# Performance work log

Measured on AMD Instinct MI355X. Metric: run time of the kernel, lower is better.

Reference implementation:

```python
import jax, jax.numpy as jnp
from jax import lax
import numpy as np

RATIOS = (0.5, 1.0, 2.0)
SCALES = (8, 16, 32)
BASE = 16
STRIDE = 16
IMG_H, IMG_W = 1024, 1024
NMS_THR = 0.7
N_IN = 6000   # eval mode (training=False)
N_OUT = 300
MIN_SIZE = 16


def _base_anchors():
    ctr = BASE / 2.0
    anc = []
    for r in RATIOS:
        for s in SCALES:
            h = BASE * s * np.sqrt(r)
            w = BASE * s * np.sqrt(1.0 / r)
            anc.append([ctr - h / 2, ctr - w / 2, ctr + h / 2, ctr + w / 2])
    return np.asarray(anc, dtype=np.float32)  # (9,4) yxyx


def _shifted_anchors(H, W):
    base = _base_anchors()
    sy = np.arange(H, dtype=np.float32) * STRIDE
    sx = np.arange(W, dtype=np.float32) * STRIDE
    yy, xx = np.meshgrid(sy, sx, indexing='ij')
    shift = np.stack([yy, xx, yy, xx], axis=-1).reshape(-1, 1, 4)  # (H*W,1,4)
    return jnp.asarray((shift + base[None]).reshape(-1, 4))        # (H*W*9,4)


def _conv(x, w, b):
    y = lax.conv_general_dilated(x, w, (1, 1), 'SAME',
                                 dimension_numbers=('NCHW', 'OIHW', 'NCHW'))
    return y + b[None, :, None, None]


def _loc2bbox(src, locs):
    h = src[:, 2] - src[:, 0]
    w = src[:, 3] - src[:, 1]
    cy = src[:, 0] + 0.5 * h
    cx = src[:, 1] + 0.5 * w
    dy, dx, dh, dw = locs[:, 0], locs[:, 1], locs[:, 2], locs[:, 3]
    cty = dy * h + cy
    ctx = dx * w + cx
    th = jnp.exp(dh) * h
    tw = jnp.exp(dw) * w
    return jnp.stack([cty - 0.5 * th, ctx - 0.5 * tw,
                      cty + 0.5 * th, ctx + 0.5 * tw], axis=-1)


def _nms_keep(boxes, valid):
    n = boxes.shape[0]
    areas = (boxes[:, 2] - boxes[:, 0]) * (boxes[:, 3] - boxes[:, 1])
    idx = jnp.arange(n)

    def body(i, keep):
        b = lax.dynamic_slice(boxes, (i, 0), (1, 4))[0]
        yy1 = jnp.maximum(b[0], boxes[:, 0])
        xx1 = jnp.maximum(b[1], boxes[:, 1])
        yy2 = jnp.minimum(b[2], boxes[:, 2])
        xx2 = jnp.minimum(b[3], boxes[:, 3])
        inter = jnp.clip(yy2 - yy1, 0) * jnp.clip(xx2 - xx1, 0)
        iou = inter / (areas[i] + areas - inter + 1e-9)
        sup = (iou > NMS_THR) & (idx > i) & keep[i]
        return keep & ~sup

    return lax.fori_loop(0, n, body, valid)


def _proposals(locs, fg, anchors):
    # locs (R,4), fg (R,), anchors (R,4) -> (N_OUT,4) padded with zeros
    rois = _loc2bbox(anchors, locs)
    y1 = jnp.clip(rois[:, 0], 0, IMG_H)
    y2 = jnp.clip(rois[:, 2], 0, IMG_H)
    x1 = jnp.clip(rois[:, 1], 0, IMG_W)
    x2 = jnp.clip(rois[:, 3], 0, IMG_W)
    rois = jnp.stack([y1, x1, y2, x2], axis=-1)
    valid = ((y2 - y1) >= MIN_SIZE) & ((x2 - x1) >= MIN_SIZE)
    s = jnp.where(valid, fg, -jnp.inf)
    order = jnp.argsort(-s)[:N_IN]
    rois_s = rois[order]
    valid_s = valid[order]
    keep = _nms_keep(rois_s, valid_s)
    rank = jnp.cumsum(keep.astype(jnp.int32)) - 1
    tgt = jnp.where(keep & (rank < N_OUT), rank, N_OUT)
    out = jnp.zeros((N_OUT + 1, 4), rois.dtype).at[tgt].set(rois_s)
    return out[:N_OUT]


def reference(x, conv_w, conv_b, score_w, score_b, loc_w, loc_b):
    B, C, H, W = x.shape
    anchors = _shifted_anchors(H, W)                      # (R,4)
    h = jax.nn.relu(_conv(x, conv_w, conv_b))             # (B,mid,H,W)
    rpn_locs = _conv(h, loc_w, loc_b).transpose(0, 2, 3, 1).reshape(B, -1, 4)
    rpn_scores = _conv(h, score_w, score_b).transpose(0, 2, 3, 1).reshape(B, -1, 2)
    fg = jax.nn.softmax(rpn_scores, axis=2)[:, :, 1]      # (B,R)
    rois = jax.vmap(_proposals, in_axes=(0, 0, None))(rpn_locs, fg, anchors)
    rois = rois.reshape(-1, 4)                            # (B*N_OUT,4)
    roi_indices = jnp.repeat(jnp.arange(B, dtype=jnp.int32), N_OUT)
    return rpn_scores, rpn_locs, rois, roi_indices, anchors


def setup_inputs() -> dict:
    key = jax.random.key(0)
    ks = jax.random.split(key, 7)
    B, Cin, Cmid, H, W = 4, 512, 512, 64, 64
    return {
        'x': jax.random.normal(ks[0], (B, Cin, H, W), jnp.float32),
        'conv_w': jax.random.normal(ks[1], (Cmid, Cin, 3, 3), jnp.float32) * 0.01,
        'conv_b': jax.random.normal(ks[2], (Cmid,), jnp.float32) * 0.01,
        'score_w': jax.random.normal(ks[3], (18, Cmid, 1, 1), jnp.float32) * 0.01,
        'score_b': jax.random.normal(ks[4], (18,), jnp.float32) * 0.01,
        'loc_w': jax.random.normal(ks[5], (36, Cmid, 1, 1), jnp.float32) * 0.01,
        'loc_b': jax.random.normal(ks[6], (36,), jnp.float32) * 0.01,
    }
```

## Files before the change

### kernel.cpp

```cpp
#include <hip/hip_runtime.h>
#include <cstdint>
#include <cmath>

namespace {
constexpr int BATCH = 4;
constexpr int CIN   = 512;
constexpr int CMID  = 512;
constexpr int HSZ   = 64, WSZ = 64, HWP = 4096;
constexpr int NA    = 36864;
constexpr int NIN_  = 6000;
constexpr int NOUT2 = 300;
constexpr int NW    = 94;

constexpr size_t O_SC  = 0;
constexpr size_t O_LC  = 294912;
constexpr size_t O_ROI = 884736;
constexpr size_t O_IDX = 889536;
constexpr size_t O_ANC = 890736;

constexpr size_t W_H    = 0;
constexpr size_t W_WHI  = 8388608;
constexpr size_t W_WLO  = 9568256;
constexpr size_t W_XSP  = 10747904;
constexpr size_t W_END_PS = 19136512;
constexpr size_t W_R4   = 0;
constexpr size_t W_SK   = 589824;
constexpr size_t W_CNT  = 753664;
constexpr size_t W_CKEY = 901184;
constexpr size_t W_RS   = 1196096;
constexpr size_t W_VS   = 1292096;
constexpr size_t W_MAT  = 1316096;
}

typedef _Float16 f16;
typedef __attribute__((ext_vector_type(4))) _Float16 f16x4;
typedef __attribute__((ext_vector_type(8))) _Float16 f16x8;
typedef __attribute__((ext_vector_type(4))) float f32x4;

__global__ __launch_bounds__(256) void k0w(const float* __restrict__ w,
                                           f16* __restrict__ whi, f16* __restrict__ wlo) {
    int o = blockIdx.x * 256 + threadIdx.x;
    int ci = o & 511;
    int r  = o >> 9;
    int co = r & 511;
    int kk = r >> 9;
    float f = w[(co * CIN + ci) * 9 + kk] * 64.0f;
    f16 hv = (f16)f;
    whi[o] = hv;
    wlo[o] = (f16)((f - (float)hv) * 2048.0f);
}

__global__ __launch_bounds__(256) void k0x(const float* __restrict__ x,
                                           f16* __restrict__ xsp) {
    const int pt = blockIdx.x, ch = blockIdx.y, b = blockIdx.z, t = threadIdx.x;
    __shared__ float ld[32 * 261];
    const int px0 = pt * 256;
    const int lpx = (t & 63) * 4, lc0 = t >> 6;
#pragma unroll
    for (int r = 0; r < 8; ++r) {
        int ci = r * 4 + lc0;
        float4 v = *(const float4*)&x[((size_t)(b * 512 + ch * 32 + ci)) * 4096 + px0 + lpx];
        float* d = &ld[ci * 261 + lpx];
        d[0] = v.x; d[1] = v.y; d[2] = v.z; d[3] = v.w;
    }
    __syncthreads();
    size_t ob = ((size_t)(b * 16 + ch) * 4096 + px0 + t) * 64;
#pragma unroll
    for (int cqx = 0; cqx < 8; ++cqx) {
        f16x8 o;
#pragma unroll
        for (int i = 0; i < 4; ++i) {
            float f = ld[(cqx * 4 + i) * 261 + t];
            f16 hf = (f16)f;
            o[i]     = hf;
            o[4 + i] = (f16)((f - (float)hf) * 2048.0f);
        }
        *(f16x8*)&xsp[ob + cqx * 8] = o;
    }
}

template <bool PS>
__global__ __launch_bounds__(256, 2) void k1_mfma(const float* __restrict__ x,
                                                  const f16* __restrict__ xsp,
                                                  const f16* __restrict__ gwh,
                                                  const f16* __restrict__ gwl,
                                                  const float* __restrict__ bias,
                                                  float* __restrict__ h) {
    const int pt = blockIdx.x, cg = blockIdx.y, b = blockIdx.z;
    const int y0 = pt * 2, co0 = cg * 128;
    const int t = threadIdx.x;
    const int wave = t >> 6, lane = t & 63;
    const int wrow = wave >> 1, wco = wave & 1;
    const int m = lane & 15, q = lane >> 4;

    __shared__ __align__(16) f16 xs[2][4 * 66 * 40];
    __shared__ __align__(16) f16 wt[2][2][128 * 32];

    f32x4 acc1[4][4], acc2[4][4];
#pragma unroll
    for (int i = 0; i < 4; ++i)
#pragma unroll
        for (int j = 0; j < 4; ++j) { acc1[i][j] = (f32x4)0.0f; acc2[i][j] = (f32x4)0.0f; }

    const int cq = t & 7, srow = (t >> 3) & 3, cseg = t >> 5;
    const int gy = y0 - 1 + srow;
    const bool yok = (gy >= 0 && gy < HSZ);

    if (t < 128) {
        int buf = t >> 6, rr = (t >> 4) & 3, cc = ((t >> 3) & 1) ? 65 : 0, cq2 = t & 7;
        f16x4 z = (f16x4)(f16)0.0f;
        *(f16x4*)&xs[buf][(rr * 66 + cc) * 40 + cq2 * 4] = z;
    }

    int wbase[2], wpos[2];
#pragma unroll
    for (int s = 0; s < 2; ++s) {
        int idx = s * 256 + t;
        int co_l = idx >> 2, q8 = idx & 3;
        wbase[s] = (co0 + co_l) * 512 + q8 * 8;
        wpos[s]  = co_l * 32 + ((q8 * 8) ^ (((co_l >> 1) & 3) << 3));
    }
#pragma unroll
    for (int s = 0; s < 2; ++s) {
        *(f16x8*)&wt[0][0][wpos[s]] = *(const f16x8*)&gwh[wbase[s]];
        *(f16x8*)&wt[0][1][wpos[s]] = *(const f16x8*)&gwl[wbase[s]];
    }

    const int baseB = wco * 2048 + m * 32 + ((q * 8) ^ (((m >> 1) & 3) << 3));

    int chunk = 0, kk = 0;
    for (int ks = 0; ks < 144; ++ks) {
        const int slot = ks & 1;
        __syncthreads();

        if (kk == 0) {
            if (PS) {
                const f16* xb = xsp + (((size_t)(b * 16 + chunk) * 4096 + (size_t)(gy < 0 ? 0 : gy) * 64) * 64);
#pragma unroll
                for (int j = 0; j < 8; ++j) {
                    int c = (j + cq) & 7;
                    int col = cseg * 8 + c + 1;
                    f16x8 v = (f16x8)(f16)0.0f;
                    if (yok) v = *(const f16x8*)&xb[(size_t)(cseg * 8 + c) * 64 + cq * 8];
                    int base = (srow * 66 + col) * 40 + cq * 4;
                    *(f16x4*)&xs[0][base] = __builtin_shufflevector(v, v, 0, 1, 2, 3);
                    *(f16x4*)&xs[1][base] = __builtin_shufflevector(v, v, 4, 5, 6, 7);
                }
            } else {
                float vb[4][8];
                const float* xp = x + ((size_t)(b * CIN + chunk * 32 + cq * 4)) * HWP + gy * WSZ + cseg * 8;
#pragma unroll
                for (int i = 0; i < 4; ++i) {
                    if (yok) {
                        float4 u0 = *(const float4*)(xp + (size_t)i * HWP);
                        float4 u1 = *(const float4*)(xp + (size_t)i * HWP + 4);
                        vb[i][0] = u0.x; vb[i][1] = u0.y; vb[i][2] = u0.z; vb[i][3] = u0.w;
                        vb[i][4] = u1.x; vb[i][5] = u1.y; vb[i][6] = u1.z; vb[i][7] = u1.w;
                    } else {
#pragma unroll
                        for (int jj = 0; jj < 8; ++jj) vb[i][jj] = 0.0f;
                    }
                }
#pragma unroll
                for (int j = 0; j < 8; ++j) {
                    int c = (j + cq) & 7;
                    int col = cseg * 8 + c + 1;
                    f16x4 hv, lv;
#pragma unroll
                    for (int i = 0; i < 4; ++i) {
                        float f = vb[i][c];
                        f16 hf = (f16)f;
                        hv[i] = hf;
                        lv[i] = (f16)((f - (float)hf) * 2048.0f);
                    }
                    int base = (srow * 66 + col) * 40 + cq * 4;
                    *(f16x4*)&xs[0][base] = hv;
                    *(f16x4*)&xs[1][base] = lv;
                }
            }
        }

        if (ks + 1 < 144) {
            int kk2 = kk + 1, ch2 = chunk;
            if (kk2 == 9) { kk2 = 0; ch2++; }
            const int gofs = kk2 * 262144 + ch2 * 32;
#pragma unroll
            for (int s = 0; s < 2; ++s) {
                int g = wbase[s] + gofs;
                *(f16x8*)&wt[slot ^ 1][0][wpos[s]] = *(const f16x8*)&gwh[g];
                *(f16x8*)&wt[slot ^ 1][1][wpos[s]] = *(const f16x8*)&gwl[g];
            }
        }

        if (kk == 0) __syncthreads();

        const int ky = (kk >= 6) ? 2 : (kk >= 3) ? 1 : 0;
        const int kx = kk - ky * 3;
        const int rs = wrow + ky;

        f16x8 bh[4], bl[4], ah[4], al[4];
#pragma unroll
        for (int nt = 0; nt < 4; ++nt) {
            int off = baseB + nt * 512;
            bh[nt] = *(const f16x8*)&wt[slot][0][off];
            bl[nt] = *(const f16x8*)&wt[slot][1][off];
        }
#pragma unroll
        for (int ct = 0; ct < 4; ++ct) {
            int off = (rs * 66 + ct * 16 + m + kx) * 40 + q * 8;
            ah[ct] = *(const f16x8*)&xs[0][off];
            al[ct] = *(const f16x8*)&xs[1][off];
        }
#pragma unroll
        for (int ct = 0; ct < 4; ++ct)
#pragma unroll
            for (int nt = 0; nt < 4; ++nt) {
                acc1[ct][nt] = __builtin_amdgcn_mfma_f32_16x16x32_f16(ah[ct], bh[nt], acc1[ct][nt], 0, 0, 0);
                acc2[ct][nt] = __builtin_amdgcn_mfma_f32_16x16x32_f16(ah[ct], bl[nt], acc2[ct][nt], 0, 0, 0);
                acc2[ct][nt] = __builtin_amdgcn_mfma_f32_16x16x32_f16(al[ct], bh[nt], acc2[ct][nt], 0, 0, 0);
            }

        ++kk;
        if (kk == 9) { kk = 0; ++chunk; }
    }

    const int y = y0 + wrow;
#pragma unroll
    for (int nt = 0; nt < 4; ++nt) {
        const int co = co0 + wco * 64 + nt * 16 + m;
        const float bv = bias[co];
        size_t rowbase = ((size_t)(b * CMID + co)) * HWP + y * WSZ;
#pragma unroll
        for (int ct = 0; ct < 4; ++ct) {
            float4 o;
            o.x = fmaxf((acc1[ct][nt][0] + acc2[ct][nt][0] * (1.0f / 2048.0f)) * (1.0f / 64.0f) + bv, 0.0f);
            o.y = fmaxf((acc1[ct][nt][1] + acc2[ct][nt][1] * (1.0f / 2048.0f)) * (1.0f / 64.0f) + bv, 0.0f);
            o.z = fmaxf((acc1[ct][nt][2] + acc2[ct][nt][2] * (1.0f / 2048.0f)) * (1.0f / 64.0f) + bv, 0.0f);
            o.w = fmaxf((acc1[ct][nt][3] + acc2[ct][nt][3] * (1.0f / 2048.0f)) * (1.0f / 64.0f) + bv, 0.0f);
            *(float4*)&h[rowbase + ct * 16 + q * 4] = o;
        }
    }
}

__global__ __launch_bounds__(256) void k2_conv1(const float* __restrict__ h,
                                                const float* __restrict__ sw,
                                                const float* __restrict__ sb,
                                                const float* __restrict__ lw,
                                                const float* __restrict__ lb,
                                                float* __restrict__ out) {
    const int y = blockIdx.x;
    const int b = blockIdx.y;
    const int t = threadIdx.x;
    const int c4  = (t & 15) * 4;
    const int px4 = (t >> 4) * 4;
    __shared__ __align__(16) float hs[1024];
    __shared__ __align__(16) float wsm[16 * 68];

    float acc[4][4];
#pragma unroll
    for (int i = 0; i < 4; ++i)
#pragma unroll
        for (int j = 0; j < 4; ++j) acc[i][j] = 0.f;

    const int s_px = (t & 15) * 4;
    const int s_ci = t >> 4;
    for (int ci0 = 0; ci0 < CMID; ci0 += 16) {
        *(float4*)&hs[s_ci * 64 + s_px] =
            *(const float4*)&h[((size_t)(b * CMID + ci0 + s_ci)) * HWP + y * 64 + s_px];
#pragma unroll
        for (int k = 0; k < 4; ++k) {
            int idx = k * 256 + t;
            int ci = idx & 15, c = idx >> 4;
            float v = 0.f;
            if (c < 18) v = sw[c * 512 + ci0 + ci];
            else if (c < 54) v = lw[(c - 18) * 512 + ci0 + ci];
            wsm[ci * 68 + c] = v;
        }
        __syncthreads();
#pragma unroll
        for (int ci = 0; ci < 16; ++ci) {
            float4 hv = *(const float4*)&hs[ci * 64 + px4];
            float4 wv = *(const float4*)&wsm[ci * 68 + c4];
            acc[0][0] = fmaf(wv.x, hv.x, acc[0][0]);
            acc[0][1] = fmaf(wv.x, hv.y, acc[0][1]);
            acc[0][2] = fmaf(wv.x, hv.z, acc[0][2]);
            acc[0][3] = fmaf(wv.x, hv.w, acc[0][3]);
            acc[1][0] = fmaf(wv.y, hv.x, acc[1][0]);
            acc[1][1] = fmaf(wv.y, hv.y, acc[1][1]);
            acc[1][2] = fmaf(wv.y, hv.z, acc[1][2]);
            acc[1][3] = fmaf(wv.y, hv.w, acc[1][3]);
            acc[2][0] = fmaf(wv.z, hv.x, acc[2][0]);
            acc[2][1] = fmaf(wv.z, hv.y, acc[2][1]);
            acc[2][2] = fmaf(wv.z, hv.z, acc[2][2]);
            acc[2][3] = fmaf(wv.z, hv.w, acc[2][3]);
            acc[3][0] = fmaf(wv.w, hv.x, acc[3][0]);
            acc[3][1] = fmaf(wv.w, hv.y, acc[3][1]);
            acc[3][2] = fmaf(wv.w, hv.z, acc[3][2]);
            acc[3][3] = fmaf(wv.w, hv.w, acc[3][3]);
        }
        __syncthreads();
    }

#pragma unroll
    for (int cc = 0; cc < 4; ++cc) {
        int c = c4 + cc;
        if (c >= 54) break;
        float bv = (c < 18) ? sb[c] : lb[c - 18];
#pragma unroll
        for (int pp = 0; pp < 4; ++pp) {
            int px = y * 64 + px4 + pp;
            float v = acc[cc][pp] + bv;
            if (c < 18)
                out[O_SC + (size_t)b * 73728 + (size_t)px * 18 + c] = v;
            else
                out[O_LC + (size_t)b * 147456 + (size_t)px * 36 + (c - 18)] = v;
        }
    }
}

__global__ __launch_bounds__(256) void k3_prop(float* __restrict__ out,
                                               float* __restrict__ rois4,
                                               float* __restrict__ skey) {
    const int t = threadIdx.x;
    const int p = blockIdx.x * 256 + t;
    const int b = blockIdx.y;
    const int px = p / 9;
    const int a  = p - px * 9;
    const int yy = px >> 6, xx = px & 63;
    const int ri = a / 3, si = a - ri * 3;
    const double rat[3] = {0.5, 1.0, 2.0};
    const double scl[3] = {8.0, 16.0, 32.0};
    double hhd = 16.0 * scl[si] * sqrt(rat[ri]);
    double wwd = 16.0 * scl[si] * sqrt(1.0 / rat[ri]);
    float a0 = (float)(8.0 - hhd / 2.0), a1 = (float)(8.0 - wwd / 2.0);
    float a2 = (float)(8.0 + hhd / 2.0), a3 = (float)(8.0 + wwd / 2.0);
    float sy = (float)(yy * 16), sx = (float)(xx * 16);
    float A0 = sy + a0, A1 = sx + a1, A2 = sy + a2, A3 = sx + a3;
    if (b == 0) {
        float4 av; av.x = A0; av.y = A1; av.z = A2; av.w = A3;
        *(float4*)&out[O_ANC + (size_t)p * 4] = av;
    }
    const float* sc = out + O_SC + (size_t)b * 73728 + (size_t)px * 18 + a * 2;
    float s0 = sc[0], s1 = sc[1];
    float mm = fmaxf(s0, s1);
    float e0 = expf(s0 - mm), e1 = expf(s1 - mm);
    float fg = e1 / (e0 + e1);
    const float* lc = out + O_LC + (size_t)b * 147456 + (size_t)px * 36 + a * 4;
    float dy = lc[0], dxv = lc[1], dh = lc[2], dwv = lc[3];
    float ah = A2 - A0, aw = A3 - A1;
    float cy = A0 + 0.5f * ah, cx = A1 + 0.5f * aw;
    float cty = dy * ah + cy, ctx = dxv * aw + cx;
    float th = expf(dh) * ah, tw = expf(dwv) * aw;
    float ry1 = cty - 0.5f * th, rx1 = ctx - 0.5f * tw;
    float ry2 = cty + 0.5f * th, rx2 = ctx + 0.5f * tw;
    float y1 = fminf(fmaxf(ry1, 0.f), 1024.f);
    float y2 = fminf(fmaxf(ry2, 0.f), 1024.f);
    float x1 = fminf(fmaxf(rx1, 0.f), 1024.f);
    float x2 = fminf(fmaxf(rx2, 0.f), 1024.f);
    bool valid = ((y2 - y1) >= 16.f) && ((x2 - x1) >= 16.f);
    float sk = valid ? fg : -__builtin_inff();
    float4 rv; rv.x = y1; rv.y = x1; rv.z = y2; rv.w = x2;
    *(float4*)&rois4[((size_t)b * NA + p) * 4] = rv;
    skey[(size_t)b * NA + p] = sk;
}

__global__ __launch_bounds__(1024) void k4rc(const float* __restrict__ skey,
                                             int* __restrict__ cnt,
                                             unsigned long long* __restrict__ ckey) {
    const int b = blockIdx.x, t = threadIdx.x;
    const int w8 = (t >> 6) & 7;
    __shared__ int h8[8][4096];
    __shared__ int tsum[256];
    __shared__ int s_cut, s_prev, lcnt;
    int cum = 0;
    int cuts[3];
#pragma unroll 1
    for (int level = 0; level < 3; ++level) {
        for (int k = t; k < 8 * 4096; k += 1024) ((int*)h8)[k] = 0;
        __syncthreads();
        for (int i = t; i < NA; i += 1024) {
            float sk = skey[(size_t)b * NA + i];
            unsigned u = __float_as_uint(sk);
            u = (u & 0x80000000u) ? ~u : (u | 0x80000000u);
            int b1 = (int)(u >> 20), b2 = (int)((u >> 8) & 0xFFFu);
            int digit; bool pred;
            if (level == 0)      { digit = b1;                pred = true; }
            else if (level == 1) { digit = b2;                pred = (b1 == cuts[0]); }
            else                 { digit = (36863 - i) >> 4;  pred = (b1 == cuts[0] && b2 == cuts[1]); }
            if (pred) atomicAdd(&h8[w8][digit], 1);
        }
        __syncthreads();
        for (int k = t; k < 4096; k += 1024) {
            int s = h8[0][k];
#pragma unroll
            for (int r = 1; r < 8; ++r) s += h8[r][k];
            h8[0][k] = s;
        }
        __syncthreads();
        if (t < 256) {
            int s = 0;
#pragma unroll
            for (int j = 0; j < 16; ++j) s += h8[0][t * 16 + j];
            tsum[t] = s;
        }
        __syncthreads();
        if (t == 0) {
            int run = 0;
            for (int tt = 255; tt >= 0; --tt) { int tmp = tsum[tt]; tsum[tt] = run; run += tmp; }
        }
        __syncthreads();
        if (t < 256) {
            const int target = NIN_ - cum;
            int run = tsum[t];
            for (int v = t * 16 + 15; v >= t * 16; --v) {
                int prev = run;
                run += h8[0][v];
                if (run >= target && prev < target) { s_cut = v; s_prev = prev; }
            }
        }
        __syncthreads();
        cuts[level] = s_cut;
        cum += s_prev;
        __syncthreads();
    }
    if (t == 0) lcnt = 0;
    __syncthreads();
    const int c1 = cuts[0], c2 = cuts[1], c3 = cuts[2];
    for (int i = t; i < NA; i += 1024) {
        float sk = skey[(size_t)b * NA + i];
        unsigned u = __float_as_uint(sk);
        u = (u & 0x80000000u) ? ~u : (u | 0x80000000u);
        int b1 = (int)(u >> 20), b2 = (int)((u >> 8) & 0xFFFu), b3 = (36863 - i) >> 4;
        bool take = (b1 > c1) || (b1 == c1 && (b2 > c2 || (b2 == c2 && b3 >= c3)));
        if (take) {
            int pos = atomicAdd(&lcnt, 1);
            ckey[(size_t)b * NA + pos] =
                ((unsigned long long)u << 16) | (unsigned long long)(36863 - i);
        }
    }
    __syncthreads();
    if (t == 0) cnt[b] = lcnt;
}

__global__ __launch_bounds__(256) void k4d_rank(const int* __restrict__ cnt,
                                                const unsigned long long* __restrict__ ckey,
                                                const float* __restrict__ rois4,
                                                float* __restrict__ rois_s,
                                                int* __restrict__ valid_s) {
    const int b = blockIdx.y;
    const int C = cnt[b];
    if (blockIdx.x * 256 >= C) return;
    const int gi = blockIdx.x * 256 + threadIdx.x;
    const bool act = gi < C;
    const unsigned long long mk = act ? ckey[(size_t)b * NA + gi] : 0ULL;
    __shared__ unsigned long long kl[512];
    int rank = 0;
    for (int c0 = 0; c0 < C; c0 += 512) {
        __syncthreads();
#pragma unroll
        for (int kk = 0; kk < 2; ++kk) {
            int k = threadIdx.x + kk * 256;
            int src = c0 + k;
            kl[k] = (src < C) ? ckey[(size_t)b * NA + src] : 0ULL;
        }
        __syncthreads();
        if (act) {
            int n = min(512, C - c0);
            int j = 0;
            for (; j + 4 <= n; j += 4) {
                rank += (kl[j]     > mk);
                rank += (kl[j + 1] > mk);
                rank += (kl[j + 2] > mk);
                rank += (kl[j + 3] > mk);
            }
            for (; j < n; ++j) rank += (kl[j] > mk);
        }
    }
    if (act && rank < NIN_) {
        int p = 36863 - (int)(mk & 0xFFFFull);
        const float4 bx = *(const float4*)&rois4[((size_t)b * NA + p) * 4];
        *(float4*)&rois_s[((size_t)b * NIN_ + rank) * 4] = bx;
        valid_s[b * NIN_ + rank] = ((unsigned)(mk >> 16) != 0x007FFFFFu) ? 1 : 0;
    }
}

__global__ __launch_bounds__(256) void k5_mat(const float* __restrict__ rois_s,
                                              unsigned long long* __restrict__ mat) {
    const int b = blockIdx.y, rb = blockIdx.x;
    const int t = threadIdx.x, wave = t >> 6, lane = t & 63;
    const int i = rb * 64 + lane;
    const bool rowok = (i < NIN_);
    __shared__ float cs[4][5][64];
    const float* bb = rois_s + (size_t)b * NIN_ * 4;

    float r0 = 0, r1 = 0, r2 = 0, r3 = 0, ra = 0;
    if (rowok) {
        float4 v = *(const float4*)&bb[(size_t)i * 4];
        r0 = v.x; r1 = v.y; r2 = v.z; r3 = v.w;
        ra = (v.z - v.x) * (v.w - v.y);
    }
    unsigned long long* mrow = mat + ((size_t)b * NIN_ + (size_t)(rowok ? i : 0)) * NW;

    if (rowok)
        for (int cb = wave; cb < rb; cb += 4) mrow[cb] = 0ull;

    for (int cb = rb + wave; cb < NW; cb += 4) {
        const int j0 = cb * 64;
        const int j  = j0 + lane;
        float4 v;
        if (j < NIN_) v = *(const float4*)&bb[(size_t)j * 4];
        else { v.x = 0; v.y = 0; v.z = 0; v.w = 0; }
        cs[wave][0][lane] = v.x; cs[wave][1][lane] = v.y;
        cs[wave][2][lane] = v.z; cs[wave][3][lane] = v.w;
        cs[wave][4][lane] = (v.z - v.x) * (v.w - v.y);
        unsigned long long wm = 0;
        if (rowok) {
#pragma unroll 8
            for (int k = 0; k < 64; ++k) {
                float yy1 = fmaxf(r0, cs[wave][0][k]), xx1 = fmaxf(r1, cs[wave][1][k]);
                float yy2 = fminf(r2, cs[wave][2][k]), xx2 = fminf(r3, cs[wave][3][k]);
                float inter = fmaxf(yy2 - yy1, 0.f) * fmaxf(xx2 - xx1, 0.f);
                float iou = inter / (ra + cs[wave][4][k] - inter + 1e-9f);
                int jj = j0 + k;
                if ((iou > 0.7f) && (jj > i) && (jj < NIN_)) wm |= (1ull << k);
            }
            mrow[cb] = wm;
        }
    }
}

__global__ __launch_bounds__(64) void k5_scan(const unsigned long long* __restrict__ mat,
                                              const float* __restrict__ rois_s,
                                              const int* __restrict__ valid_s,
                                              float* __restrict__ out) {
    const int b = blockIdx.x, t = threadIdx.x;
    for (int k = t; k < NOUT2 * 4; k += 64) out[O_ROI + (size_t)b * NOUT2 * 4 + k] = 0.f;
    for (int k = t; k < NOUT2; k += 64) out[O_IDX + (size_t)b * NOUT2 + k] = (float)b;

    unsigned long long A = 0, B = 0;
    for (int w = 0; w < NW; ++w) {
        int i = w * 64 + t;
        int v = (i < NIN_) ? valid_s[b * NIN_ + i] : 0;
        unsigned long long m = __ballot(v == 0);
        if (w < 64) { if (t == w) A = m; }
        else        { if (t == w - 64) B = m; }
    }

    const unsigned long long* mb = mat + (size_t)b * NIN_ * NW;
    const float* bb = rois_s + (size_t)b * NIN_ * 4;
    int kept = 0;
    for (int w = 0; w < NW && kept < NOUT2; ++w) {
        unsigned long long cur = (w < 64) ? __shfl(A, w) : __shfl(B, w - 64);
        unsigned long long avail = ~cur;
        while (avail != 0ull && kept < NOUT2) {
            int bit = __builtin_ctzll(avail);
            int i = w * 64 + bit;
            if (t == 0) {
                float4 bx = *(const float4*)&bb[(size_t)i * 4];
                *(float4*)&out[O_ROI + ((size_t)b * NOUT2 + kept) * 4] = bx;
            }
            kept++;
            if (kept >= NOUT2) break;
            const unsigned long long* row = mb + (size_t)i * NW;
            unsigned long long rA = row[t];
            unsigned long long rB = (t < NW - 64) ? row[64 + t] : 0ull;
            A |= rA; B |= rB;
            unsigned long long rw = (w < 64) ? __shfl(rA, w) : __shfl(rB, w - 64);
            avail &= ~rw;
            avail &= ~(1ull << bit);
        }
    }
}

extern "C" void kernel_launch(void* const* d_in, const int* in_sizes, int n_in,
                              void* d_out, int out_size, void* d_ws, size_t ws_size,
                              hipStream_t stream) {
    const float* x       = (const float*)d_in[0];
    const float* conv_w  = (const float*)d_in[1];
    const float* conv_b  = (const float*)d_in[2];
    const float* score_w = (const float*)d_in[3];
    const float* score_b = (const float*)d_in[4];
    const float* loc_w   = (const float*)d_in[5];
    const float* loc_b   = (const float*)d_in[6];
    float* out = (float*)d_out;
    float* ws  = (float*)d_ws;

    f16* whi = (f16*)(ws + W_WHI);
    f16* wlo = (f16*)(ws + W_WLO);
    f16* xsp = (f16*)(ws + W_XSP);
    const bool ps = (ws_size >= (size_t)W_END_PS * 4);

    k0w<<<2359296 / 256, 256, 0, stream>>>(conv_w, whi, wlo);
    if (ps) {
        k0x<<<dim3(16, 16, 4), 256, 0, stream>>>(x, xsp);
        k1_mfma<true><<<dim3(32, 4, 4), 256, 0, stream>>>(x, xsp, whi, wlo, conv_b, ws + W_H);
    } else {
        k1_mfma<false><<<dim3(32, 4, 4), 256, 0, stream>>>(x, nullptr, whi, wlo, conv_b, ws + W_H);
    }
    k2_conv1<<<dim3(64, 4), 256, 0, stream>>>(ws + W_H, score_w, score_b, loc_w, loc_b, out);
    k3_prop<<<dim3(144, 4), 256, 0, stream>>>(out, ws + W_R4, ws + W_SK);
    k4rc<<<BATCH, 1024, 0, stream>>>(ws + W_SK, (int*)(ws + W_CNT),
                                     (unsigned long long*)(ws + W_CKEY));
    k4d_rank<<<dim3(24, BATCH), 256, 0, stream>>>((const int*)(ws + W_CNT),
                                                  (const unsigned long long*)(ws + W_CKEY),
                                                  ws + W_R4, ws + W_RS, (int*)(ws + W_VS));
    k5_mat<<<dim3(NW, BATCH), 256, 0, stream>>>(ws + W_RS, (unsigned long long*)(ws + W_MAT));
    k5_scan<<<BATCH, 64, 0, stream>>>((const unsigned long long*)(ws + W_MAT),
                                      ws + W_RS, (const int*)(ws + W_VS), out);
}
```

Before: 887.5 us.

## Pre-swizzle weights into MFMA fragment layout and load B operands directly from global

The weight prep kernel now writes hi/lo f16 weights into one interleaved buffer in the exact per-lane MFMA fragment order, so the conv kernel drops its shared-memory weight staging and double-buffered barriers. Each wave instead reads B fragments straight from global/L2 per kernel tap. Waves now cover 2 rows x 2 column tiles rather than 1 row x 4. The change also aggregates histogram atomics with a ballot-based warp grouping, and adds speculative prefetch of upcoming NMS mask rows. The risks are higher global load latency in the MFMA loop with no software pipelining, and extra wasted loads in the NMS scan.

```diff
diff --git a/kernel.cpp b/kernel.cpp
--- a/kernel.cpp
+++ b/kernel.cpp
@@ -38,16 +38,27 @@
 typedef __attribute__((ext_vector_type(4))) float f32x4;
 
 __global__ __launch_bounds__(256) void k0w(const float* __restrict__ w,
-                                           f16* __restrict__ whi, f16* __restrict__ wlo) {
-    int o = blockIdx.x * 256 + threadIdx.x;
-    int ci = o & 511;
-    int r  = o >> 9;
-    int co = r & 511;
-    int kk = r >> 9;
-    float f = w[(co * CIN + ci) * 9 + kk] * 64.0f;
-    f16 hv = (f16)f;
-    whi[o] = hv;
-    wlo[o] = (f16)((f - (float)hv) * 2048.0f);
+                                           f16* __restrict__ gw2) {
+    int g = blockIdx.x * 256 + threadIdx.x;
+    int lane = g & 63;
+    int t1 = g >> 6;
+    int hl = t1 & 1;
+    int nt = (t1 >> 1) & 3;
+    int wc = (t1 >> 3) & 1;
+    int cg = (t1 >> 4) & 3;
+    int ck = t1 >> 6;
+    int kk = ck % 9;
+    int chunk = ck / 9;
+    int co  = cg * 128 + wc * 64 + nt * 16 + (lane & 15);
+    int ci0 = chunk * 32 + (lane >> 4) * 8;
+    f16x8 o;
+#pragma unroll
+    for (int e = 0; e < 8; ++e) {
+        float f = w[((size_t)co * CIN + ci0 + e) * 9 + kk] * 64.0f;
+        f16 hv = (f16)f;
+        o[e] = hl ? (f16)((f - (float)hv) * 2048.0f) : hv;
+    }
+    *(f16x8*)&gw2[(size_t)g * 8] = o;
 }
 
 __global__ __launch_bounds__(256) void k0x(const float* __restrict__ x,
@@ -82,25 +93,25 @@
 template <bool PS>
 __global__ __launch_bounds__(256, 2) void k1_mfma(const float* __restrict__ x,
                                                   const f16* __restrict__ xsp,
-                                                  const f16* __restrict__ gwh,
-                                                  const f16* __restrict__ gwl,
+                                                  const f16* __restrict__ gw2,
                                                   const float* __restrict__ bias,
                                                   float* __restrict__ h) {
     const int pt = blockIdx.x, cg = blockIdx.y, b = blockIdx.z;
     const int y0 = pt * 2, co0 = cg * 128;
     const int t = threadIdx.x;
     const int wave = t >> 6, lane = t & 63;
-    const int wrow = wave >> 1, wco = wave & 1;
+    const int wp = wave >> 1, wc = wave & 1;
     const int m = lane & 15, q = lane >> 4;
 
     __shared__ __align__(16) f16 xs[2][4 * 66 * 40];
-    __shared__ __align__(16) f16 wt[2][2][128 * 32];
-
-    f32x4 acc1[4][4], acc2[4][4];
-#pragma unroll
-    for (int i = 0; i < 4; ++i)
-#pragma unroll
-        for (int j = 0; j < 4; ++j) { acc1[i][j] = (f32x4)0.0f; acc2[i][j] = (f32x4)0.0f; }
+
+    f32x4 acc1[2][2][4], acc2[2][2][4];
+#pragma unroll
+    for (int r = 0; r < 2; ++r)
+#pragma unroll
+        for (int j = 0; j < 2; ++j)
+#pragma unroll
+            for (int n = 0; n < 4; ++n) { acc1[r][j][n] = (f32x4)0.0f; acc2[r][j][n] = (f32x4)0.0f; }
 
     const int cq = t & 7, srow = (t >> 3) & 3, cseg = t >> 5;
     const int gy = y0 - 1 + srow;
@@ -112,132 +123,107 @@
         *(f16x4*)&xs[buf][(rr * 66 + cc) * 40 + cq2 * 4] = z;
     }
 
-    int wbase[2], wpos[2];
-#pragma unroll
-    for (int s = 0; s < 2; ++s) {
-        int idx = s * 256 + t;
-        int co_l = idx >> 2, q8 = idx & 3;
-        wbase[s] = (co0 + co_l) * 512 + q8 * 8;
-        wpos[s]  = co_l * 32 + ((q8 * 8) ^ (((co_l >> 1) & 3) << 3));
-    }
-#pragma unroll
-    for (int s = 0; s < 2; ++s) {
-        *(f16x8*)&wt[0][0][wpos[s]] = *(const f16x8*)&gwh[wbase[s]];
-        *(f16x8*)&wt[0][1][wpos[s]] = *(const f16x8*)&gwl[wbase[s]];
-    }
-
-    const int baseB = wco * 2048 + m * 32 + ((q * 8) ^ (((m >> 1) & 3) << 3));
-
-    int chunk = 0, kk = 0;
-    for (int ks = 0; ks < 144; ++ks) {
-        const int slot = ks & 1;
-        __syncthreads();
-
-        if (kk == 0) {
-            if (PS) {
-                const f16* xb = xsp + (((size_t)(b * 16 + chunk) * 4096 + (size_t)(gy < 0 ? 0 : gy) * 64) * 64);
-#pragma unroll
-                for (int j = 0; j < 8; ++j) {
-                    int c = (j + cq) & 7;
-                    int col = cseg * 8 + c + 1;
-                    f16x8 v = (f16x8)(f16)0.0f;
-                    if (yok) v = *(const f16x8*)&xb[(size_t)(cseg * 8 + c) * 64 + cq * 8];
-                    int base = (srow * 66 + col) * 40 + cq * 4;
-                    *(f16x4*)&xs[0][base] = __builtin_shufflevector(v, v, 0, 1, 2, 3);
-                    *(f16x4*)&xs[1][base] = __builtin_shufflevector(v, v, 4, 5, 6, 7);
+    const size_t wlanebase = (size_t)(cg * 2 + wc) * 4096 + (size_t)lane * 8;
+
+    for (int chunk = 0; chunk < 16; ++chunk) {
+        __syncthreads();
+        if (PS) {
+            const f16* xb = xsp + (((size_t)(b * 16 + chunk) * 4096 + (size_t)(yok ? gy : 0) * 64) * 64);
+#pragma unroll
+            for (int jj = 0; jj < 8; ++jj) {
+                int c = (jj + cq) & 7;
+                int col = cseg * 8 + c + 1;
+                f16x8 v = (f16x8)(f16)0.0f;
+                if (yok) v = *(const f16x8*)&xb[(size_t)(cseg * 8 + c) * 64 + cq * 8];
+                int base = (srow * 66 + col) * 40 + cq * 4;
+                *(f16x4*)&xs[0][base] = __builtin_shufflevector(v, v, 0, 1, 2, 3);
+                *(f16x4*)&xs[1][base] = __builtin_shufflevector(v, v, 4, 5, 6, 7);
+            }
+        } else {
+            float vbuf[4][8];
+            const float* xp = x + ((size_t)(b * CIN + chunk * 32 + cq * 4)) * HWP + gy * WSZ + cseg * 8;
+#pragma unroll
+            for (int i = 0; i < 4; ++i) {
+                if (yok) {
+                    float4 u0 = *(const float4*)(xp + (size_t)i * HWP);
+                    float4 u1 = *(const float4*)(xp + (size_t)i * HWP + 4);
+                    vbuf[i][0] = u0.x; vbuf[i][1] = u0.y; vbuf[i][2] = u0.z; vbuf[i][3] = u0.w;
+                    vbuf[i][4] = u1.x; vbuf[i][5] = u1.y; vbuf[i][6] = u1.z; vbuf[i][7] = u1.w;
+                } else {
+#pragma unroll
+                    for (int jj = 0; jj < 8; ++jj) vbuf[i][jj] = 0.0f;
                 }
-            } else {
-                float vb[4][8];
-                const float* xp = x + ((size_t)(b * CIN + chunk * 32 + cq * 4)) * HWP + gy * WSZ + cseg * 8;
+            }
+#pragma unroll
+            for (int jj = 0; jj < 8; ++jj) {
+                int c = (jj + cq) & 7;
+                int col = cseg * 8 + c + 1;
+                f16x4 hv, lv;
 #pragma unroll
                 for (int i = 0; i < 4; ++i) {
-                    if (yok) {
-                        float4 u0 = *(const float4*)(xp + (size_t)i * HWP);
-                        float4 u1 = *(const float4*)(xp + (size_t)i * HWP + 4);
-                        vb[i][0] = u0.x; vb[i][1] = u0.y; vb[i][2] = u0.z; vb[i][3] = u0.w;
-                        vb[i][4] = u1.x; vb[i][5] = u1.y; vb[i][6] = u1.z; vb[i][7] = u1.w;
-                    } else {
-#pragma unroll
-                        for (int jj = 0; jj < 8; ++jj) vb[i][jj] = 0.0f;
+                    float f = vbuf[i][c];
+                    f16 hf = (f16)f;
+                    hv[i] = hf;
+                    lv[i] = (f16)((f - (float)hf) * 2048.0f);
+                }
+                int base = (srow * 66 + col) * 40 + cq * 4;
+                *(f16x4*)&xs[0][base] = hv;
+                *(f16x4*)&xs[1][base] = lv;
+            }
+        }
+        __syncthreads();
+
+        const f16* wck = gw2 + (size_t)chunk * (9 * 32768) + wlanebase;
+#pragma unroll
+        for (int kk = 0; kk < 9; ++kk) {
+            const int ky = (kk >= 6) ? 2 : (kk >= 3) ? 1 : 0;
+            const int kx = kk - ky * 3;
+            const f16* wptr = wck + (size_t)kk * 32768;
+            f16x8 bh[4], bl[4];
+#pragma unroll
+            for (int nt = 0; nt < 4; ++nt) {
+                bh[nt] = *(const f16x8*)&wptr[nt * 1024];
+                bl[nt] = *(const f16x8*)&wptr[nt * 1024 + 512];
+            }
+            f16x8 ah[2][2], al[2][2];
+#pragma unroll
+            for (int r = 0; r < 2; ++r)
+#pragma unroll
+                for (int j = 0; j < 2; ++j) {
+                    int off = ((r + ky) * 66 + (wp * 2 + j) * 16 + m + kx) * 40 + q * 8;
+                    ah[r][j] = *(const f16x8*)&xs[0][off];
+                    al[r][j] = *(const f16x8*)&xs[1][off];
+                }
+#pragma unroll
+            for (int r = 0; r < 2; ++r)
+#pragma unroll
+                for (int j = 0; j < 2; ++j)
+#pragma unroll
+                    for (int nt = 0; nt < 4; ++nt) {
+                        acc1[r][j][nt] = __builtin_amdgcn_mfma_f32_16x16x32_f16(ah[r][j], bh[nt], acc1[r][j][nt], 0, 0, 0);
+                        acc2[r][j][nt] = __builtin_amdgcn_mfma_f32_16x16x32_f16(ah[r][j], bl[nt], acc2[r][j][nt], 0, 0, 0);
+                        acc2[r][j][nt] = __builtin_amdgcn_mfma_f32_16x16x32_f16(al[r][j], bh[nt], acc2[r][j][nt], 0, 0, 0);
                     }
-                }
-#pragma unroll
-                for (int j = 0; j < 8; ++j) {
-                    int c = (j + cq) & 7;
-                    int col = cseg * 8 + c + 1;
-                    f16x4 hv, lv;
-#pragma unroll
-                    for (int i = 0; i < 4; ++i) {
-                        float f = vb[i][c];
-                        f16 hf = (f16)f;
-                        hv[i] = hf;
-                        lv[i] = (f16)((f - (float)hf) * 2048.0f);
-                    }
-                    int base = (srow * 66 + col) * 40 + cq * 4;
-                    *(f16x4*)&xs[0][base] = hv;
-                    *(f16x4*)&xs[1][base] = lv;
-                }
-            }
-        }
-
-        if (ks + 1 < 144) {
-            int kk2 = kk + 1, ch2 = chunk;
-            if (kk2 == 9) { kk2 = 0; ch2++; }
-            const int gofs = kk2 * 262144 + ch2 * 32;
-#pragma unroll
-            for (int s = 0; s < 2; ++s) {
-                int g = wbase[s] + gofs;
-                *(f16x8*)&wt[slot ^ 1][0][wpos[s]] = *(const f16x8*)&gwh[g];
-                *(f16x8*)&wt[slot ^ 1][1][wpos[s]] = *(const f16x8*)&gwl[g];
-            }
-        }
-
-        if (kk == 0) __syncthreads();
-
-        const int ky = (kk >= 6) ? 2 : (kk >= 3) ? 1 : 0;
-        const int kx = kk - ky * 3;
-        const int rs = wrow + ky;
-
-        f16x8 bh[4], bl[4], ah[4], al[4];
+        }
+    }
+
+#pragma unroll
+    for (int r = 0; r < 2; ++r) {
+        const int y = y0 + r;
 #pragma unroll
         for (int nt = 0; nt < 4; ++nt) {
-            int off = baseB + nt * 512;
-            bh[nt] = *(const f16x8*)&wt[slot][0][off];
-            bl[nt] = *(const f16x8*)&wt[slot][1][off];
-        }
-#pragma unroll
-        for (int ct = 0; ct < 4; ++ct) {
-            int off = (rs * 66 + ct * 16 + m + kx) * 40 + q * 8;
-            ah[ct] = *(const f16x8*)&xs[0][off];
-            al[ct] = *(const f16x8*)&xs[1][off];
-        }
-#pragma unroll
-        for (int ct = 0; ct < 4; ++ct)
-#pragma unroll
-            for (int nt = 0; nt < 4; ++nt) {
-                acc1[ct][nt] = __builtin_amdgcn_mfma_f32_16x16x32_f16(ah[ct], bh[nt], acc1[ct][nt], 0, 0, 0);
-                acc2[ct][nt] = __builtin_amdgcn_mfma_f32_16x16x32_f16(ah[ct], bl[nt], acc2[ct][nt], 0, 0, 0);
-                acc2[ct][nt] = __builtin_amdgcn_mfma_f32_16x16x32_f16(al[ct], bh[nt], acc2[ct][nt], 0, 0, 0);
-            }
-
-        ++kk;
-        if (kk == 9) { kk = 0; ++chunk; }
-    }
-
-    const int y = y0 + wrow;
-#pragma unroll
-    for (int nt = 0; nt < 4; ++nt) {
-        const int co = co0 + wco * 64 + nt * 16 + m;
-        const float bv = bias[co];
-        size_t rowbase = ((size_t)(b * CMID + co)) * HWP + y * WSZ;
-#pragma unroll
-        for (int ct = 0; ct < 4; ++ct) {
-            float4 o;
-            o.x = fmaxf((acc1[ct][nt][0] + acc2[ct][nt][0] * (1.0f / 2048.0f)) * (1.0f / 64.0f) + bv, 0.0f);
-            o.y = fmaxf((acc1[ct][nt][1] + acc2[ct][nt][1] * (1.0f / 2048.0f)) * (1.0f / 64.0f) + bv, 0.0f);
-            o.z = fmaxf((acc1[ct][nt][2] + acc2[ct][nt][2] * (1.0f / 2048.0f)) * (1.0f / 64.0f) + bv, 0.0f);
-            o.w = fmaxf((acc1[ct][nt][3] + acc2[ct][nt][3] * (1.0f / 2048.0f)) * (1.0f / 64.0f) + bv, 0.0f);
-            *(float4*)&h[rowbase + ct * 16 + q * 4] = o;
+            const int co = co0 + wc * 64 + nt * 16 + m;
+            const float bv = bias[co];
+            size_t rowbase = ((size_t)(b * CMID + co)) * HWP + y * WSZ;
+#pragma unroll
+            for (int j = 0; j < 2; ++j) {
+                float4 o;
+                o.x = fmaxf((acc1[r][j][nt][0] + acc2[r][j][nt][0] * (1.0f / 2048.0f)) * (1.0f / 64.0f) + bv, 0.0f);
+                o.y = fmaxf((acc1[r][j][nt][1] + acc2[r][j][nt][1] * (1.0f / 2048.0f)) * (1.0f / 64.0f) + bv, 0.0f);
+                o.z = fmaxf((acc1[r][j][nt][2] + acc2[r][j][nt][2] * (1.0f / 2048.0f)) * (1.0f / 64.0f) + bv, 0.0f);
+                o.w = fmaxf((acc1[r][j][nt][3] + acc2[r][j][nt][3] * (1.0f / 2048.0f)) * (1.0f / 64.0f) + bv, 0.0f);
+                *(float4*)&h[rowbase + (wp * 2 + j) * 16 + q * 4] = o;
+            }
         }
     }
 }
@@ -369,6 +355,7 @@
                                              unsigned long long* __restrict__ ckey) {
     const int b = blockIdx.x, t = threadIdx.x;
     const int w8 = (t >> 6) & 7;
+    const int ln = t & 63;
     __shared__ int h8[8][4096];
     __shared__ int tsum[256];
     __shared__ int s_cut, s_prev, lcnt;
@@ -387,7 +374,16 @@
             if (level == 0)      { digit = b1;                pred = true; }
             else if (level == 1) { digit = b2;                pred = (b1 == cuts[0]); }
             else                 { digit = (36863 - i) >> 4;  pred = (b1 == cuts[0] && b2 == cuts[1]); }
-            if (pred) atomicAdd(&h8[w8][digit], 1);
+            bool need = pred;
+            while (__any(need)) {
+                unsigned long long msk = __ballot(need);
+                int leader = (int)__builtin_ctzll(msk);
+                int ldig = __shfl(digit, leader);
+                bool mine = need && (digit == ldig);
+                unsigned long long grp = __ballot(mine);
+                if (ln == leader) atomicAdd(&h8[w8][ldig], (int)__builtin_popcountll(grp));
+                need = need && !mine;
+            }
         }
         __syncthreads();
         for (int k = t; k < 4096; k += 1024) {
@@ -555,6 +551,20 @@
         while (avail != 0ull && kept < NOUT2) {
             int bit = __builtin_ctzll(avail);
             int i = w * 64 + bit;
+            {
+                unsigned long long spec = avail & (avail - 1);
+#pragma unroll
+                for (int pf = 0; pf < 2; ++pf) {
+                    if (spec != 0ull) {
+                        int nb = __builtin_ctzll(spec);
+                        const unsigned long long* pr = mb + (size_t)(w * 64 + nb) * NW;
+                        unsigned long long j1 = pr[t];
+                        unsigned long long j2 = (t < NW - 64) ? pr[64 + t] : 0ull;
+                        asm volatile("" :: "v"(j1), "v"(j2));
+                        spec &= spec - 1;
+                    }
+                }
+            }
             if (t == 0) {
                 float4 bx = *(const float4*)&bb[(size_t)i * 4];
                 *(float4*)&out[O_ROI + ((size_t)b * NOUT2 + kept) * 4] = bx;
@@ -585,17 +595,16 @@
     float* out = (float*)d_out;
     float* ws  = (float*)d_ws;
 
-    f16* whi = (f16*)(ws + W_WHI);
-    f16* wlo = (f16*)(ws + W_WLO);
+    f16* gw2 = (f16*)(ws + W_WHI);
     f16* xsp = (f16*)(ws + W_XSP);
     const bool ps = (ws_size >= (size_t)W_END_PS * 4);
 
-    k0w<<<2359296 / 256, 256, 0, stream>>>(conv_w, whi, wlo);
+    k0w<<<589824 / 256, 256, 0, stream>>>(conv_w, gw2);
     if (ps) {
         k0x<<<dim3(16, 16, 4), 256, 0, stream>>>(x, xsp);
-        k1_mfma<true><<<dim3(32, 4, 4), 256, 0, stream>>>(x, xsp, whi, wlo, conv_b, ws + W_H);
+        k1_mfma<true><<<dim3(32, 4, 4), 256, 0, stream>>>(x, xsp, gw2, conv_b, ws + W_H);
     } else {
-        k1_mfma<false><<<dim3(32, 4, 4), 256, 0, stream>>>(x, nullptr, whi, wlo, conv_b, ws + W_H);
+        k1_mfma<false><<<dim3(32, 4, 4), 256, 0, stream>>>(x, nullptr, gw2, conv_b, ws + W_H);
     }
     k2_conv1<<<dim3(64, 4), 256, 0, stream>>>(ws + W_H, score_w, score_b, loc_w, loc_b, out);
     k3_prop<<<dim3(144, 4), 256, 0, stream>>>(out, ws + W_R4, ws + W_SK);
```

New measurement: 1.138 ms. +28.2%, slower.
